# Optimization experiments

Measured on AMD Instinct MI355X. Metric: run time of the kernel, lower is better.

## Reference

```python
import jax, jax.numpy as jnp
import numpy as np

TEMPERATURE = 1.0

def _cauchy_kernel(x, y, temperature):
    # pairwise squared distances via Gram trick: ||x_i - y_j||^2
    sq_x = jnp.sum(x * x, axis=1)  # [n]
    sq_y = jnp.sum(y * y, axis=1)  # [m]
    d2 = sq_x[:, None] + sq_y[None, :] - 2.0 * (x @ y.T)
    d2 = jnp.maximum(d2, 0.0)
    return 1.0 / (1.0 + d2 / temperature)


def setup_inputs() -> dict:
    key = jax.random.key(0)
    k1, k2 = jax.random.split(key)
    features = jax.random.normal(k1, (8192, 128), dtype=jnp.float32)
    labels = jax.random.randint(k2, (8192,), 0, 1000, dtype=jnp.int64)
    return {"features": features, "labels": labels}


def reference(features, labels):
    b = features.shape[0] // 2
    z1 = features[:b]
    z2 = features[b:]
    z11 = _cauchy_kernel(z1, z1, TEMPERATURE)  # [b,b]
    z22 = _cauchy_kernel(z2, z2, TEMPERATURE)  # [b,b]
    z12 = _cauchy_kernel(z1, z2, TEMPERATURE)  # [b,b]

    eye = jnp.eye(b, dtype=z11.dtype)
    # positive term: mean log of matched-pair kernel (diagonal of z12)
    pos = jnp.sum(jnp.log(jnp.diagonal(z12))) / b
    # negative terms: row sums over [z11 - I | z12] and [z12^T | z22 - I]
    n1 = jnp.mean(jnp.log((z11 - eye).sum(axis=1) + z12.sum(axis=1)))
    n2 = jnp.mean(jnp.log(z12.sum(axis=0) + (z22 - eye).sum(axis=1)))
    neg = (n1 + n2) / 2.0
    return -(pos - neg)
```

## Files before the change

kernel.cpp:

```cpp
#include <hip/hip_runtime.h>
#include <math.h>

#define N_TOTAL 8192
#define BHALF   4096
#define KDIM    128
#define NTILE   64
#define NTRI    2080
#define NBLK_PW 512

typedef __bf16 bf16x8 __attribute__((ext_vector_type(8)));
typedef __bf16 bf16x2 __attribute__((ext_vector_type(2)));
typedef float  f32x4  __attribute__((ext_vector_type(4)));

#define GLOAD_LDS16(GSRC, LDST)                                                \
    __builtin_amdgcn_global_load_lds(                                          \
        (const __attribute__((address_space(1))) void*)(GSRC),                 \
        (__attribute__((address_space(3))) void*)(LDST), 16, 0, 0)

template <int CTRL>
__device__ __forceinline__ float dpp_add(float x) {
    union { float f; int i; } u, v;
    u.f = x;
    v.i = __builtin_amdgcn_update_dpp(0, u.i, CTRL, 0xF, 0xF, true);
    return x + v.f;
}

__global__ __launch_bounds__(256) void k_prep_pos(const float* __restrict__ F,
                                                  __bf16* __restrict__ Fbf,
                                                  float* __restrict__ sq,
                                                  float* __restrict__ posPart,
                                                  float* __restrict__ out) {
    int t = threadIdx.x;
    int w = t >> 6, l = t & 63;
    int p = blockIdx.x * 4 + w;
    const float2* r1 = (const float2*)(F + (size_t)p * KDIM);
    const float2* r2 = (const float2*)(F + (size_t)(p + BHALF) * KDIM);
    float2 a = r1[l];
    float2 c = r2[l];

    float s1 = fmaf(a.x, a.x, a.y * a.y);
    float s2 = fmaf(c.x, c.x, c.y * c.y);
    float dp = fmaf(a.x, c.x, a.y * c.y);
#pragma unroll
    for (int off = 32; off > 0; off >>= 1) {
        s1 += __shfl_down(s1, off);
        s2 += __shfl_down(s2, off);
        dp += __shfl_down(dp, off);
    }

    bf16x2 pa, pc;
    pa[0] = (__bf16)a.x; pa[1] = (__bf16)a.y;
    pc[0] = (__bf16)c.x; pc[1] = (__bf16)c.y;
    ((bf16x2*)(Fbf + (size_t)p * KDIM))[l] = pa;
    ((bf16x2*)(Fbf + (size_t)(p + BHALF) * KDIM))[l] = pc;

    __shared__ float posRed[4];
    if (l == 0) {
        sq[p] = s1;
        sq[p + BHALF] = s2;
        float d2 = fmaxf(s1 + s2 - 2.0f * dp, 0.0f);
        posRed[w] = logf(1.0f + d2);
    }
    __syncthreads();
    if (t == 0) {
        posPart[blockIdx.x] = posRed[0] + posRed[1] + posRed[2] + posRed[3];
        if (blockIdx.x == 0) out[0] = 0.0f;
    }
}

__global__ __launch_bounds__(512, 4) void k_pairwise(
        const __bf16* __restrict__ Fbf,
        const float* __restrict__ sq,
        float* __restrict__ Tpart) {
    __shared__ __align__(16) __bf16 As[128 * 128];
    __shared__ __align__(16) __bf16 Bs[128 * 128];
    __shared__ float rowAcc[128][2];
    __shared__ float colAcc[128][4];

    int t = threadIdx.x;
    int w = t >> 6;
    int l = t & 63;
    int wr = w >> 1, wc = w & 1;
    int low = l & 15, kb = l >> 4;

    int bid = blockIdx.x;
    int start = bid * 4 + (bid < 32 ? bid : 32);
    int cnt = (bid < 32) ? 5 : 4;

    int ti = (int)floorf((129.0f - sqrtf(16641.0f - 8.0f * (float)start)) * 0.5f);
    while (ti * (129 - ti) / 2 > start) --ti;
    while ((ti + 1) * (128 - ti) / 2 <= start) ++ti;
    int tj = ti + (start - ti * (129 - ti) / 2);

    auto stage = [&](const __bf16* src, __bf16* dst) {
#pragma unroll
        for (int it = 0; it < 4; ++it) {
            int f = it * 512 + t;
            int row = f >> 4;
            int sg = f & 15;
            int g = sg ^ (row & 15);
            GLOAD_LDS16(src + row * KDIM + g * 8, dst + (size_t)f * 8);
        }
    };

    int curTi = -1;
#pragma unroll 1
    for (int n = 0; n < cnt; ++n) {
        int I = ti * 128, J = tj * 128;
        bool diag = (ti == tj);

        if (ti != curTi) {
            stage(Fbf + (size_t)I * KDIM, As);
            curTi = ti;
        }
        if (!diag) {
            stage(Fbf + (size_t)J * KDIM, Bs);
        }
        __syncthreads();

        const bf16x8* Asg = (const bf16x8*)As;
        const bf16x8* Bsg = diag ? (const bf16x8*)As : (const bf16x8*)Bs;
        f32x4 acc[2][4] = {};
#pragma unroll
        for (int s = 0; s < 4; ++s) {
            int g = s * 4 + kb;
            bf16x8 aF[2], bF[4];
#pragma unroll
            for (int fr = 0; fr < 2; ++fr) {
                int R = wr * 32 + fr * 16 + low;
                aF[fr] = Asg[R * 16 + (g ^ low)];
            }
#pragma unroll
            for (int fc = 0; fc < 4; ++fc) {
                int C = wc * 64 + fc * 16 + low;
                bF[fc] = Bsg[C * 16 + (g ^ low)];
            }
#pragma unroll
            for (int fr = 0; fr < 2; ++fr)
#pragma unroll
                for (int fc = 0; fc < 4; ++fc)
                    acc[fr][fc] = __builtin_amdgcn_mfma_f32_16x16x32_bf16(
                        aF[fr], bF[fc], acc[fr][fc], 0, 0, 0);
        }

        float sqi1[2][4], sqj[4];
#pragma unroll
        for (int fr = 0; fr < 2; ++fr)
#pragma unroll
            for (int r = 0; r < 4; ++r)
                sqi1[fr][r] = 1.0f + sq[I + wr * 32 + fr * 16 + kb * 4 + r];
#pragma unroll
        for (int fc = 0; fc < 4; ++fc)
            sqj[fc] = sq[J + wc * 64 + fc * 16 + low];

        f32x4 rowPart[2] = {};
        float colPart[4] = {0.f, 0.f, 0.f, 0.f};
#pragma unroll
        for (int fr = 0; fr < 2; ++fr) {
#pragma unroll
            for (int fc = 0; fc < 4; ++fc) {
                f32x4 vv;
#pragma unroll
                for (int r = 0; r < 4; ++r) {
                    float d2 = fmaf(acc[fr][fc][r], -2.0f,
                                    sqi1[fr][r] + sqj[fc]);
                    vv[r] = __builtin_amdgcn_rcpf(fmaxf(d2, 1.0f));
                }
                rowPart[fr] += vv;
                colPart[fc] += (vv[0] + vv[1]) + (vv[2] + vv[3]);
            }
        }

#pragma unroll
        for (int fr = 0; fr < 2; ++fr)
#pragma unroll
            for (int r = 0; r < 4; ++r) {
                float x = rowPart[fr][r];
                x = dpp_add<0xB1>(x);
                x = dpp_add<0x4E>(x);
                x = dpp_add<0x141>(x);
                x = dpp_add<0x140>(x);
                if (low == 0)
                    rowAcc[wr * 32 + fr * 16 + kb * 4 + r][wc] = x;
            }

#pragma unroll
        for (int fc = 0; fc < 4; ++fc) {
            float x = colPart[fc];
            x += __shfl_xor(x, 16);
            x += __shfl_xor(x, 32);
            if (kb == 0)
                colAcc[wc * 64 + fc * 16 + low][wr] = x;
        }
        __syncthreads();

        if (t < 128) {
            Tpart[tj * N_TOTAL + I + t] = rowAcc[t][0] + rowAcc[t][1];
        } else if (t < 256 && !diag) {
            int c = t - 128;
            Tpart[ti * N_TOTAL + J + c] =
                colAcc[c][0] + colAcc[c][1] + colAcc[c][2] + colAcc[c][3];
        }

        ++tj;
        if (tj == NTILE) { ++ti; tj = ti; }
    }
}

__global__ __launch_bounds__(256) void k_final(const float* __restrict__ Tpart,
                                               const float* __restrict__ posPart,
                                               float* __restrict__ out) {
    int t = threadIdx.x;
    int i = blockIdx.x * 256 + t;
    float s = 0.0f;
#pragma unroll 8
    for (int k = 0; k < NTILE; ++k) s += Tpart[k * N_TOTAL + i];
    float v = logf(s - 1.0f);
    if (t < 32) v += 2.0f * posPart[blockIdx.x * 32 + t];
#pragma unroll
    for (int off = 32; off > 0; off >>= 1) v += __shfl_down(v, off);
    __shared__ float red[4];
    int w = t >> 6, l = t & 63;
    if (l == 0) red[w] = v;
    __syncthreads();
    if (t == 0) {
        float S = red[0] + red[1] + red[2] + red[3];
        atomicAdd(out, S * (1.0f / (2.0f * (float)BHALF)));
    }
}

extern "C" void kernel_launch(void* const* d_in, const int* in_sizes, int n_in,
                              void* d_out, int out_size, void* d_ws, size_t ws_size,
                              hipStream_t stream) {
    const float* F = (const float*)d_in[0];
    float* out = (float*)d_out;

    char* ws = (char*)d_ws;
    __bf16* Fbf     = (__bf16*)ws;
    float*  sq      = (float*)(ws + (size_t)N_TOTAL * KDIM * 2);
    float*  posPart = sq + N_TOTAL;
    float*  Tpart   = posPart + 1024;

    k_prep_pos<<<BHALF / 4, 256, 0, stream>>>(F, Fbf, sq, posPart, out);
    k_pairwise<<<NBLK_PW, 512, 0, stream>>>(Fbf, sq, Tpart);
    k_final<<<N_TOTAL / 256, 256, 0, stream>>>(Tpart, posPart, out);
}
```

Measured before the change: 82.52 us.

## Fuse final log-reduction into pairwise kernel via per-tile completion counters

Drops the separate final kernel. Each pairwise block bumps per-row-tile atomic counters once it has written its partial row sums. The block that completes a tile then reduces that tile's 64 partials, applies the log and positive term, and atomically adds the result to the output. The column-sum cross-lane reduction also switches from two shuffles to a permlane32 swap, with a wider LDS staging array. This saves one launch and the tail of a dependent kernel, at the cost of extra atomics, fences and a serialized reduction on the last-finishing blocks.

New measurement: 166.5 us. +101.8%, slower.

```diff
diff --git a/kernel.cpp b/kernel.cpp
--- a/kernel.cpp
+++ b/kernel.cpp
@@ -11,6 +11,7 @@
 typedef __bf16 bf16x8 __attribute__((ext_vector_type(8)));
 typedef __bf16 bf16x2 __attribute__((ext_vector_type(2)));
 typedef float  f32x4  __attribute__((ext_vector_type(4)));
+typedef unsigned u32x2 __attribute__((ext_vector_type(2)));
 
 #define GLOAD_LDS16(GSRC, LDST)                                                \
     __builtin_amdgcn_global_load_lds(                                          \
@@ -25,10 +26,19 @@
     return x + v.f;
 }
 
+__device__ __forceinline__ float permlane32_sum(float x) {
+    union { float f; unsigned u; } a; a.f = x;
+    u32x2 r = __builtin_amdgcn_permlane32_swap(a.u, a.u, false, false);
+    union { unsigned u; float f; } b0, b1;
+    b0.u = r[0]; b1.u = r[1];
+    return b0.f + b1.f;
+}
+
 __global__ __launch_bounds__(256) void k_prep_pos(const float* __restrict__ F,
                                                   __bf16* __restrict__ Fbf,
                                                   float* __restrict__ sq,
                                                   float* __restrict__ posPart,
+                                                  unsigned* __restrict__ cnt,
                                                   float* __restrict__ out) {
     int t = threadIdx.x;
     int w = t >> 6, l = t & 63;
@@ -38,6 +48,8 @@
     float2 a = r1[l];
     float2 c = r2[l];
 
+    if (blockIdx.x == 0 && t < 64) cnt[t] = 0u;
+
     float s1 = fmaf(a.x, a.x, a.y * a.y);
     float s2 = fmaf(c.x, c.x, c.y * c.y);
     float dp = fmaf(a.x, c.x, a.y * c.y);
@@ -71,11 +83,17 @@
 __global__ __launch_bounds__(512, 4) void k_pairwise(
         const __bf16* __restrict__ Fbf,
         const float* __restrict__ sq,
-        float* __restrict__ Tpart) {
+        float* __restrict__ Tpart,
+        const float* __restrict__ posPart,
+        unsigned* __restrict__ cnt,
+        float* __restrict__ out) {
     __shared__ __align__(16) __bf16 As[128 * 128];
     __shared__ __align__(16) __bf16 Bs[128 * 128];
     __shared__ float rowAcc[128][2];
-    __shared__ float colAcc[128][4];
+    __shared__ float colAcc[128][8];
+    __shared__ int finList[12];
+    __shared__ int nFin;
+    __shared__ float red2[2];
 
     int t = threadIdx.x;
     int w = t >> 6;
@@ -85,12 +103,13 @@
 
     int bid = blockIdx.x;
     int start = bid * 4 + (bid < 32 ? bid : 32);
-    int cnt = (bid < 32) ? 5 : 4;
+    int cnt_n = (bid < 32) ? 5 : 4;
 
     int ti = (int)floorf((129.0f - sqrtf(16641.0f - 8.0f * (float)start)) * 0.5f);
     while (ti * (129 - ti) / 2 > start) --ti;
     while ((ti + 1) * (128 - ti) / 2 <= start) ++ti;
     int tj = ti + (start - ti * (129 - ti) / 2);
+    int ti0 = ti, tj0 = tj;
 
     auto stage = [&](const __bf16* src, __bf16* dst) {
 #pragma unroll
@@ -105,7 +124,7 @@
 
     int curTi = -1;
 #pragma unroll 1
-    for (int n = 0; n < cnt; ++n) {
+    for (int n = 0; n < cnt_n; ++n) {
         int I = ti * 128, J = tj * 128;
         bool diag = (ti == tj);
 
@@ -186,11 +205,9 @@
 
 #pragma unroll
         for (int fc = 0; fc < 4; ++fc) {
-            float x = colPart[fc];
-            x += __shfl_xor(x, 16);
-            x += __shfl_xor(x, 32);
-            if (kb == 0)
-                colAcc[wc * 64 + fc * 16 + low][wr] = x;
+            float x = permlane32_sum(colPart[fc]);
+            if (l < 32)
+                colAcc[wc * 64 + fc * 16 + low][wr * 2 + kb] = x;
         }
         __syncthreads();
 
@@ -198,34 +215,63 @@
             Tpart[tj * N_TOTAL + I + t] = rowAcc[t][0] + rowAcc[t][1];
         } else if (t < 256 && !diag) {
             int c = t - 128;
+            const float* ca = colAcc[c];
             Tpart[ti * N_TOTAL + J + c] =
-                colAcc[c][0] + colAcc[c][1] + colAcc[c][2] + colAcc[c][3];
+                ((ca[0] + ca[1]) + (ca[2] + ca[3])) +
+                ((ca[4] + ca[5]) + (ca[6] + ca[7]));
         }
 
         ++tj;
         if (tj == NTILE) { ++ti; tj = ti; }
     }
-}
-
-__global__ __launch_bounds__(256) void k_final(const float* __restrict__ Tpart,
-                                               const float* __restrict__ posPart,
-                                               float* __restrict__ out) {
-    int t = threadIdx.x;
-    int i = blockIdx.x * 256 + t;
-    float s = 0.0f;
-#pragma unroll 8
-    for (int k = 0; k < NTILE; ++k) s += Tpart[k * N_TOTAL + i];
-    float v = logf(s - 1.0f);
-    if (t < 32) v += 2.0f * posPart[blockIdx.x * 32 + t];
-#pragma unroll
-    for (int off = 32; off > 0; off >>= 1) v += __shfl_down(v, off);
-    __shared__ float red[4];
-    int w = t >> 6, l = t & 63;
-    if (l == 0) red[w] = v;
+
     __syncthreads();
+    __threadfence();
     if (t == 0) {
-        float S = red[0] + red[1] + red[2] + red[3];
-        atomicAdd(out, S * (1.0f / (2.0f * (float)BHALF)));
+        int nf = 0;
+        int a = ti0, b = tj0;
+        for (int n = 0; n < cnt_n; ++n) {
+            unsigned c = atomicAdd(&cnt[a], 1u);
+            if (c == 63u) finList[nf++] = a;
+            if (a != b) {
+                c = atomicAdd(&cnt[b], 1u);
+                if (c == 63u) finList[nf++] = b;
+            }
+            ++b; if (b == NTILE) { ++a; b = a; }
+        }
+        nFin = nf;
+    }
+    __syncthreads();
+    int nf = nFin;
+    if (nf == 0) return;
+    __threadfence();
+
+    int e = t & 127, q = t >> 7;
+#pragma unroll 1
+    for (int f = 0; f < nf; ++f) {
+        int g = finList[f];
+        const float* col = Tpart + (size_t)g * 128 + e;
+        float s = 0.f;
+#pragma unroll
+        for (int k = 0; k < 16; ++k)
+            s += col[(size_t)(q * 16 + k) * N_TOTAL];
+        colAcc[e][q] = s;
+        __syncthreads();
+        float v = 0.f;
+        if (t < 128) {
+            float ssum = colAcc[t][0] + colAcc[t][1] +
+                         colAcc[t][2] + colAcc[t][3];
+            v = logf(ssum - 1.0f);
+            if (t < 32 && g < 32)
+                v += 2.0f * posPart[g * 32 + t];
+#pragma unroll
+            for (int off = 32; off > 0; off >>= 1) v += __shfl_down(v, off);
+            if ((t & 63) == 0) red2[t >> 6] = v;
+        }
+        __syncthreads();
+        if (t == 0)
+            atomicAdd(out, (red2[0] + red2[1]) * (1.0f / (2.0f * (float)BHALF)));
+        __syncthreads();
     }
 }
 
@@ -240,8 +286,8 @@
     float*  sq      = (float*)(ws + (size_t)N_TOTAL * KDIM * 2);
     float*  posPart = sq + N_TOTAL;
     float*  Tpart   = posPart + 1024;
-
-    k_prep_pos<<<BHALF / 4, 256, 0, stream>>>(F, Fbf, sq, posPart, out);
-    k_pairwise<<<NBLK_PW, 512, 0, stream>>>(Fbf, sq, Tpart);
-    k_final<<<N_TOTAL / 256, 256, 0, stream>>>(Tpart, posPart, out);
-}
+    unsigned* cnt   = (unsigned*)(Tpart + (size_t)NTILE * N_TOTAL);
+
+    k_prep_pos<<<BHALF / 4, 256, 0, stream>>>(F, Fbf, sq, posPart, cnt, out);
+    k_pairwise<<<NBLK_PW, 512, 0, stream>>>(Fbf, sq, Tpart, posPart, cnt, out);
+}
```
